# Kernel tuning notes

Measured on AMD Instinct MI355X. Metric: run time of the kernel, lower is better.

Reference implementation:

```python
import jax, jax.numpy as jnp
import numpy as np

N_NODES = 100000
NUM_FEATURES = 512
HIDDEN = 128
OUT = 2
N_EDGES = 1600000


def setup_inputs() -> dict:
    key = jax.random.key(0)
    k_x, k_e, k_w1, k_b1, k_w2, k_b2 = jax.random.split(key, 6)
    x = jax.random.normal(k_x, (N_NODES, NUM_FEATURES), dtype=jnp.float32)
    edge_index = jax.random.randint(k_e, (2, N_EDGES), 0, N_NODES, dtype=jnp.int64)
    # GCNConv weight (Glorot-style scale) and bias
    w1 = jax.random.normal(k_w1, (NUM_FEATURES, HIDDEN), dtype=jnp.float32) / np.sqrt(NUM_FEATURES)
    b1 = jnp.zeros((HIDDEN,), dtype=jnp.float32)
    # nn.Linear weight/bias
    w2 = jax.random.normal(k_w2, (HIDDEN, OUT), dtype=jnp.float32) / np.sqrt(HIDDEN)
    b2 = jnp.zeros((OUT,), dtype=jnp.float32)
    return {"x": x, "w1": w1, "b1": b1, "w2": w2, "b2": b2, "edge_index": edge_index}


def _gcn_conv(x, edge_index, w, b, num_nodes):
    """PyG GCNConv: h = D^{-1/2} (A+I) D^{-1/2} (x @ w) + b."""
    h = x @ w  # [N, hidden] -- transform before propagate (PyG order)
    loops = jnp.arange(num_nodes, dtype=edge_index.dtype)
    src = jnp.concatenate([edge_index[0], loops])  # [E+N]
    dst = jnp.concatenate([edge_index[1], loops])
    # symmetric normalization: deg computed over destination (col) incl. self-loops
    deg = jnp.zeros((num_nodes,), dtype=h.dtype).at[dst].add(1.0)
    dinv = jax.lax.rsqrt(deg)  # deg >= 1 thanks to self-loops
    norm = dinv[src] * dinv[dst]  # [E+N]
    msg = h[src] * norm[:, None]  # gather + scale, [E+N, hidden]
    out = jax.ops.segment_sum(msg, dst, num_segments=num_nodes)  # scatter-add
    return out + b


def reference(x, w1, b1, w2, b2, edge_index):
    h = _gcn_conv(x, edge_index, w1, b1, N_NODES)  # [N, hidden]
    return h @ w2 + b2  # [N, out]
```

## Files before the change

kernel.cpp:

```cpp
#include <hip/hip_runtime.h>

constexpr int N_NODES = 100000;
constexpr int N_FEAT  = 512;
constexpr int N_EDGES = 1600000;

constexpr float FXS = 1048576.0f;
constexpr float FXB = 32.0f;

constexpr int BSH    = 8;
constexpr int BINW   = 1 << BSH;
constexpr int NBINS  = (N_NODES + BINW - 1) >> BSH;
constexpr int NSH    = 8;
constexpr int BCAP_S = 768;
constexpr int NBB    = 500;
constexpr int CHUNK  = N_EDGES / NBB;
constexpr int GRID   = 2048;
constexpr int NRB    = GRID - NBB;
constexpr int NCUR   = NBINS * NSH;

typedef float vfloat4 __attribute__((ext_vector_type(4)));

constexpr int WS_W    = 0;
constexpr int WS_C    = 1024;
constexpr int WS_CUR  = 1056;
constexpr int WS_DEG  = WS_CUR + 3200;
constexpr int WS_DINV = WS_DEG + N_NODES;
constexpr int WS_G    = WS_DINV + N_NODES;
constexpr int WS_FXP  = WS_G + 2 * N_NODES;
constexpr int WS_BINS = WS_FXP + 2 * N_NODES;

static_assert((WS_G * 4) % 8 == 0, "g alignment");
static_assert((WS_FXP * 4) % 8 == 0, "fxp alignment");
static_assert(N_NODES % 4 == 0, "");

__global__ void k_prep(const float* __restrict__ w1, const float* __restrict__ w2,
                       const float* __restrict__ b1, const float* __restrict__ b2,
                       float* __restrict__ ws) {
    int i = blockIdx.x * blockDim.x + threadIdx.x;
    if (i < NCUR) reinterpret_cast<int*>(ws + WS_CUR)[i] = 0;
    if (i < N_FEAT) {
        float a0 = 0.f, a1 = 0.f;
        for (int m = 0; m < 128; ++m) {
            float w = w1[i * 128 + m];
            a0 += w * w2[m * 2 + 0];
            a1 += w * w2[m * 2 + 1];
        }
        ws[WS_W + i] = a0;
        ws[WS_W + 512 + i] = a1;
        if (i < 2) {
            float s = b2[i];
            for (int m = 0; m < 128; ++m) s += b1[m] * w2[m * 2 + i];
            ws[WS_C + i] = s;
        }
    }
}

__global__ __launch_bounds__(256) void k_fused(
    const float* __restrict__ x, float* __restrict__ ws,
    const int* __restrict__ src, const int* __restrict__ dst,
    float2* __restrict__ g) {
    int b = blockIdx.x;
    int tid = threadIdx.x;

    __shared__ vfloat4 Wlds[256];

    if (b < NBB) {
        __shared__ int cnt[NBINS];
        __shared__ int offs[NBINS];
        __shared__ int cur2[NBINS];
        int sg = b & (NSH - 1);
        for (int i = tid; i < NBINS; i += 256) { cnt[i] = 0; cur2[i] = 0; }
        __syncthreads();
        int base = b * CHUNK;
        for (int e = base + tid; e < base + CHUNK; e += 256)
            atomicAdd(&cnt[dst[e] >> BSH], 1);
        __syncthreads();
        int* gcur = reinterpret_cast<int*>(ws + WS_CUR);
        for (int i = tid; i < NBINS; i += 256) {
            int c = cnt[i];
            int pos = c ? atomicAdd(&gcur[i * NSH + sg], c) : 0;
            offs[i] = (i * NSH + sg) * BCAP_S + pos;
        }
        __syncthreads();
        unsigned int* bins = reinterpret_cast<unsigned int*>(ws + WS_BINS);
        for (int e = base + tid; e < base + CHUNK; e += 256) {
            int d = dst[e], s = src[e];
            int bin = d >> BSH;
            int r = atomicAdd(&cur2[bin], 1);
            bins[offs[bin] + r] = (unsigned int)s | ((unsigned int)(d & (BINW - 1)) << 17);
        }
        return;
    }
    {
        const vfloat4* Wq = reinterpret_cast<const vfloat4*>(ws + WS_W);
        if (tid < 256) Wlds[tid] = Wq[tid];
        __syncthreads();
    }
    int rb = b - NBB;
    int lane = tid & 63;
    int wave = tid >> 6;
    int j = lane & 15, i4 = lane >> 4;
    const vfloat4* W0l = Wlds;
    const vfloat4* W1l = Wlds + 128;

    int wid = rb * 4 + wave;
    int nw  = NRB * 4;
    constexpr int NQ = N_NODES / 4;
    for (int q = wid; q < NQ; q += nw) {
        int row = q * 4 + i4;
        const vfloat4* xr = reinterpret_cast<const vfloat4*>(x + (size_t)row * N_FEAT);
        vfloat4 xv[8];
        #pragma unroll
        for (int k = 0; k < 8; ++k)
            xv[k] = xr[k * 16 + j];
        float a0 = 0.f, a1 = 0.f;
        #pragma unroll
        for (int k = 0; k < 8; ++k) {
            vfloat4 w0 = W0l[k * 16 + j];
            vfloat4 w1 = W1l[k * 16 + j];
            a0 += xv[k].x*w0.x + xv[k].y*w0.y + xv[k].z*w0.z + xv[k].w*w0.w;
            a1 += xv[k].x*w1.x + xv[k].y*w1.y + xv[k].z*w1.z + xv[k].w*w1.w;
        }
        #pragma unroll
        for (int off = 1; off <= 8; off <<= 1) {
            a0 += __shfl_xor(a0, off);
            a1 += __shfl_xor(a1, off);
        }
        if (j == 0) g[row] = make_float2(a0, a1);
    }
}

__global__ __launch_bounds__(512) void k_deg(float* __restrict__ ws) {
    int b = blockIdx.x;
    int tid = threadIdx.x;
    const int* gcur = reinterpret_cast<const int*>(ws + WS_CUR);
    const unsigned int* bins = reinterpret_cast<const unsigned int*>(ws + WS_BINS);
    __shared__ int cnt[BINW];
    if (tid < BINW) cnt[tid] = 0;
    __syncthreads();
    #pragma unroll
    for (int sg = 0; sg < NSH; ++sg) {
        int cell = b * NSH + sg;
        int n = min(gcur[cell], BCAP_S);
        const unsigned int* bb = bins + (size_t)cell * BCAP_S;
        for (int i = tid; i < n; i += 512)
            atomicAdd(&cnt[bb[i] >> 17], 1);
    }
    __syncthreads();
    int d = (b << BSH) + tid;
    if (tid < BINW && d < N_NODES) {
        int dg = cnt[tid] + 1;
        reinterpret_cast<int*>(ws + WS_DEG)[d] = dg;
        float di = rsqrtf((float)dg);
        ws[WS_DINV + d] = di;
        float2 gv = reinterpret_cast<const float2*>(ws + WS_G)[d];
        unsigned int lo = (unsigned int)__float2int_rn((gv.x * di + FXB) * FXS);
        unsigned int hi = (unsigned int)__float2int_rn((gv.y * di + FXB) * FXS);
        reinterpret_cast<unsigned long long*>(ws + WS_FXP)[d] =
            ((unsigned long long)hi << 32) | (unsigned long long)lo;
    }
}

__global__ __launch_bounds__(512) void k_pass2(float* __restrict__ ws,
                                               float2* __restrict__ out) {
    int b = blockIdx.x;
    int tid = threadIdx.x;
    const int* gcur = reinterpret_cast<const int*>(ws + WS_CUR);
    const unsigned int* bins = reinterpret_cast<const unsigned int*>(ws + WS_BINS);
    const int* deg = reinterpret_cast<const int*>(ws + WS_DEG);
    const float* dinv = ws + WS_DINV;
    const unsigned long long* fxp = reinterpret_cast<const unsigned long long*>(ws + WS_FXP);
    __shared__ unsigned long long acc[BINW];
    if (tid < BINW) acc[tid] = 0ull;
    __syncthreads();
    #pragma unroll
    for (int sg = 0; sg < NSH; ++sg) {
        int cell = b * NSH + sg;
        int n = min(gcur[cell], BCAP_S);
        const unsigned int* bb = bins + (size_t)cell * BCAP_S;
        for (int i = tid; i < n; i += 512) {
            unsigned int p = bb[i];
            atomicAdd(&acc[p >> 17], fxp[p & 0x1FFFFu]);
        }
    }
    __syncthreads();
    int d = (b << BSH) + tid;
    if (tid < BINW && d < N_NODES) {
        unsigned long long a = acc[tid] + fxp[d];
        long long dg = (long long)deg[d];
        long long bias = dg << 25;
        long long lo = (long long)(a & 0xFFFFFFFFull) - bias;
        long long hi = (long long)(a >> 32) - bias;
        float di = dinv[d];
        out[d] = make_float2(di * ((float)lo * (1.0f / FXS)) + ws[WS_C + 0],
                             di * ((float)hi * (1.0f / FXS)) + ws[WS_C + 1]);
    }
}

extern "C" void kernel_launch(void* const* d_in, const int* in_sizes, int n_in,
                              void* d_out, int out_size, void* d_ws, size_t ws_size,
                              hipStream_t stream) {
    const float* x  = (const float*)d_in[0];
    const float* w1 = (const float*)d_in[1];
    const float* b1 = (const float*)d_in[2];
    const float* w2 = (const float*)d_in[3];
    const float* b2 = (const float*)d_in[4];
    const int*   ei = (const int*)d_in[5];
    float* ws = (float*)d_ws;

    float2* g = (float2*)(ws + WS_G);

    k_prep<<<13, 256, 0, stream>>>(w1, w2, b1, b2, ws);
    k_fused<<<GRID, 256, 0, stream>>>(x, ws, ei, ei + N_EDGES, g);
    k_deg<<<NBINS, 512, 0, stream>>>(ws);
    k_pass2<<<NBINS, 512, 0, stream>>>(ws, (float2*)d_out);
}
```

Baseline: 79.91 us.

## Tile x@W rows per block with LDS reduction; unroll pass2 gather loop

The row-reduction branch of the fused kernel now processes 16-row tiles per block. Each thread holds a fixed column of the combined weights in registers, streams contiguous x with fully coalesced loads, and writes partial products to LDS. A second phase reduces each row across lanes, replacing the per-wave 4-row scheme and its LDS weight lookups. Separately, the pass2 scatter loop is unrolled by two so that two fxp gathers are in flight before the atomics. Costs are two block barriers per tile and extra LDS traffic, and the shared buffer is now aliased with the binning arrays.

```diff
diff --git a/kernel.cpp b/kernel.cpp
--- a/kernel.cpp
+++ b/kernel.cpp
@@ -18,6 +18,12 @@
 constexpr int NRB    = GRID - NBB;
 constexpr int NCUR   = NBINS * NSH;
 
+constexpr int TROWS  = 16;
+constexpr int NTILE  = N_NODES / TROWS;
+constexpr int TSPLIT = NTILE - NRB * 4;
+static_assert(TSPLIT >= 0 && TSPLIT < NRB, "tile split");
+constexpr int SCR_STRIDE = 136;
+
 typedef float vfloat4 __attribute__((ext_vector_type(4)));
 
 constexpr int WS_W    = 0;
@@ -31,7 +37,6 @@
 
 static_assert((WS_G * 4) % 8 == 0, "g alignment");
 static_assert((WS_FXP * 4) % 8 == 0, "fxp alignment");
-static_assert(N_NODES % 4 == 0, "");
 
 __global__ void k_prep(const float* __restrict__ w1, const float* __restrict__ w2,
                        const float* __restrict__ b1, const float* __restrict__ b2,
@@ -62,12 +67,12 @@
     int b = blockIdx.x;
     int tid = threadIdx.x;
 
-    __shared__ vfloat4 Wlds[256];
+    __shared__ __align__(16) char smem[2 * TROWS * SCR_STRIDE * 4];
 
     if (b < NBB) {
-        __shared__ int cnt[NBINS];
-        __shared__ int offs[NBINS];
-        __shared__ int cur2[NBINS];
+        int* cnt  = reinterpret_cast<int*>(smem);
+        int* offs = cnt + NBINS;
+        int* cur2 = offs + NBINS;
         int sg = b & (NSH - 1);
         for (int i = tid; i < NBINS; i += 256) { cnt[i] = 0; cur2[i] = 0; }
         __syncthreads();
@@ -91,42 +96,53 @@
         }
         return;
     }
-    {
-        const vfloat4* Wq = reinterpret_cast<const vfloat4*>(ws + WS_W);
-        if (tid < 256) Wlds[tid] = Wq[tid];
-        __syncthreads();
-    }
+
+    float (*scrA)[SCR_STRIDE] = reinterpret_cast<float (*)[SCR_STRIDE]>(smem);
+    float (*scrB)[SCR_STRIDE] =
+        reinterpret_cast<float (*)[SCR_STRIDE]>(smem + TROWS * SCR_STRIDE * 4);
+
     int rb = b - NBB;
-    int lane = tid & 63;
-    int wave = tid >> 6;
-    int j = lane & 15, i4 = lane >> 4;
-    const vfloat4* W0l = Wlds;
-    const vfloat4* W1l = Wlds + 128;
-
-    int wid = rb * 4 + wave;
-    int nw  = NRB * 4;
-    constexpr int NQ = N_NODES / 4;
-    for (int q = wid; q < NQ; q += nw) {
-        int row = q * 4 + i4;
-        const vfloat4* xr = reinterpret_cast<const vfloat4*>(x + (size_t)row * N_FEAT);
+    int t0, tcnt;
+    if (rb < TSPLIT) { t0 = rb * 5;                     tcnt = 5; }
+    else             { t0 = TSPLIT * 5 + (rb - TSPLIT) * 4; tcnt = 4; }
+
+    int c = tid & 127;
+    int row_lo = tid >> 7;
+    const vfloat4* Wq = reinterpret_cast<const vfloat4*>(ws + WS_W);
+    vfloat4 w0c = Wq[c];
+    vfloat4 w1c = Wq[128 + c];
+
+    int lane16 = tid & 15;
+    int rrow   = tid >> 4;
+
+    for (int tt = t0; tt < t0 + tcnt; ++tt) {
+        int r0 = tt * TROWS;
+        const vfloat4* xq = reinterpret_cast<const vfloat4*>(x) + (size_t)r0 * 128;
         vfloat4 xv[8];
         #pragma unroll
-        for (int k = 0; k < 8; ++k)
-            xv[k] = xr[k * 16 + j];
-        float a0 = 0.f, a1 = 0.f;
+        for (int i = 0; i < 8; ++i)
+            xv[i] = xq[i * 256 + tid];
         #pragma unroll
-        for (int k = 0; k < 8; ++k) {
-            vfloat4 w0 = W0l[k * 16 + j];
-            vfloat4 w1 = W1l[k * 16 + j];
-            a0 += xv[k].x*w0.x + xv[k].y*w0.y + xv[k].z*w0.z + xv[k].w*w0.w;
-            a1 += xv[k].x*w1.x + xv[k].y*w1.y + xv[k].z*w1.z + xv[k].w*w1.w;
-        }
+        for (int i = 0; i < 8; ++i) {
+            float pa = xv[i].x*w0c.x + xv[i].y*w0c.y + xv[i].z*w0c.z + xv[i].w*w0c.w;
+            float pb = xv[i].x*w1c.x + xv[i].y*w1c.y + xv[i].z*w1c.z + xv[i].w*w1c.w;
+            scrA[2 * i + row_lo][c] = pa;
+            scrB[2 * i + row_lo][c] = pb;
+        }
+        __syncthreads();
+        const float4* rA = reinterpret_cast<const float4*>(&scrA[rrow][0]);
+        const float4* rB = reinterpret_cast<const float4*>(&scrB[rrow][0]);
+        float4 aq0 = rA[lane16 * 2], aq1 = rA[lane16 * 2 + 1];
+        float4 bq0 = rB[lane16 * 2], bq1 = rB[lane16 * 2 + 1];
+        float sa = aq0.x + aq0.y + aq0.z + aq0.w + aq1.x + aq1.y + aq1.z + aq1.w;
+        float sb = bq0.x + bq0.y + bq0.z + bq0.w + bq1.x + bq1.y + bq1.z + bq1.w;
         #pragma unroll
         for (int off = 1; off <= 8; off <<= 1) {
-            a0 += __shfl_xor(a0, off);
-            a1 += __shfl_xor(a1, off);
-        }
-        if (j == 0) g[row] = make_float2(a0, a1);
+            sa += __shfl_xor(sa, off);
+            sb += __shfl_xor(sb, off);
+        }
+        if (lane16 == 0) g[r0 + rrow] = make_float2(sa, sb);
+        __syncthreads();
     }
 }
 
@@ -178,7 +194,15 @@
         int cell = b * NSH + sg;
         int n = min(gcur[cell], BCAP_S);
         const unsigned int* bb = bins + (size_t)cell * BCAP_S;
-        for (int i = tid; i < n; i += 512) {
+        int i = tid;
+        for (; i + 512 < n; i += 1024) {
+            unsigned int p0 = bb[i], p1 = bb[i + 512];
+            unsigned long long v0 = fxp[p0 & 0x1FFFFu];
+            unsigned long long v1 = fxp[p1 & 0x1FFFFu];
+            atomicAdd(&acc[p0 >> 17], v0);
+            atomicAdd(&acc[p1 >> 17], v1);
+        }
+        if (i < n) {
             unsigned int p = bb[i];
             atomicAdd(&acc[p >> 17], fxp[p & 0x1FFFFu]);
         }
```

New measurement: 77.70 us (median of 2 runs). 1.03x faster.
